# Kernel tuning notes

Hardware: AMD Instinct MI355X
Metric: run time of the kernel (lower is better)

## Reference

```python
import jax, jax.numpy as jnp
import numpy as np

EPS = 1e-5  # BatchNorm eps (torch default)

def _bn(x, mean, var, gamma, beta):
    # eval-mode BatchNorm over the trailing (heads, ch) axes
    return (x - mean) * (gamma / jnp.sqrt(var + EPS)) + beta

def setup_inputs() -> dict:
    key = jax.random.key(0)
    ks = jax.random.split(key, 8)
    B, C, W, H = 16, 256, 64, 64
    heads, k, u, m = 4, 16, 1, 23
    vv = 256
    kh, vh = k // heads, vv // heads
    x = jax.random.normal(ks[0], (B, C, W, H), dtype=jnp.float32)
    q_w = jax.random.normal(ks[1], (heads, kh, C), dtype=jnp.float32) * 0.05
    k_w = jax.random.normal(ks[2], (heads, kh * u, C), dtype=jnp.float32) * 0.05
    v_w = jax.random.normal(ks[3], (heads, vh * u, C), dtype=jnp.float32) * 0.05
    q_gamma = 0.5 + jax.random.uniform(ks[4], (heads, kh), dtype=jnp.float32)
    q_beta = jax.random.normal(ks[5], (heads, kh), dtype=jnp.float32) * 0.1
    q_mean = jnp.zeros((heads, kh), dtype=jnp.float32)
    q_var = jnp.ones((heads, kh), dtype=jnp.float32)
    k_gamma = 0.5 + jax.random.uniform(ks[6], (heads, kh * u), dtype=jnp.float32)
    k_beta = jax.random.normal(ks[7], (heads, kh * u), dtype=jnp.float32) * 0.1
    k_mean = jnp.zeros((heads, kh * u), dtype=jnp.float32)
    k_var = jnp.ones((heads, kh * u), dtype=jnp.float32)
    embedding = jax.random.normal(jax.random.fold_in(key, 99), (kh, heads, u, 1, m, m), dtype=jnp.float32) * 0.05
    return {"x": x, "q_w": q_w, "q_gamma": q_gamma, "q_beta": q_beta, "q_mean": q_mean,
            "q_var": q_var, "k_w": k_w, "k_gamma": k_gamma, "k_beta": k_beta,
            "k_mean": k_mean, "k_var": k_var, "v_w": v_w, "embedding": embedding}

def reference(x, q_w, q_gamma, q_beta, q_mean, q_var, k_w, k_gamma, k_beta, k_mean, k_var, v_w, embedding):
    B, C, W, H = x.shape
    heads, kh, _ = q_w.shape
    u = embedding.shape[2]
    m = embedding.shape[-1]
    vh = v_w.shape[1] // u
    pad = (m - 1) // 2

    # 1x1 conv projections (all heads stacked) -> channels-last
    q = jnp.einsum('bcxy,hkc->bxyhk', x, q_w)                      # [B,W,H,heads,kh]
    q = _bn(q, q_mean, q_var, q_gamma, q_beta)
    kk = jnp.einsum('bcxy,hkc->bxyhk', x, k_w)                     # [B,W,H,heads,kh*u]
    kk = _bn(kk, k_mean, k_var, k_gamma, k_beta)
    # softmax over all spatial positions, per (head, key-channel)
    sm = jax.nn.softmax(kk.reshape(B, W * H, heads, kh * u), axis=1)
    sm = sm.reshape(B, W, H, heads, kh, u)                          # [B,W,H,h,kh,u]
    v = jnp.einsum('bcxy,hvc->bxyhv', x, v_w).reshape(B, W, H, heads, vh, u)

    # content lambda: sum over all spatial positions
    lambda_c = jnp.einsum('bxyhku,bxyhvu->bhkv', sm, v)             # [B,h,kh,vh]
    y_c = jnp.einsum('bxyhk,bhkv->bxyhv', q, lambda_c)              # [B,W,H,h,vh]

    # positional lambda via grouped 2D conv (conv3d kernel depth is 1 -> 2D conv per vh slice)
    v_conv = v.transpose(0, 4, 3, 5, 1, 2).reshape(B * vh, heads * u, W, H)
    w = jnp.squeeze(embedding, axis=3).transpose(1, 0, 2, 3, 4).reshape(heads * kh, u, m, m)
    conv = jax.lax.conv_general_dilated(
        v_conv, w, window_strides=(1, 1), padding=[(pad, pad), (pad, pad)],
        dimension_numbers=('NCHW', 'OIHW', 'NCHW'), feature_group_count=heads)
    # [B*vh, heads*kh, W, H] -> sum over spatial (matches .sum(dim=[1,2]) in source)
    lambda_p = conv.reshape(B, vh, heads, kh, W, H).sum(axis=(4, 5))
    lambda_p = lambda_p.transpose(0, 2, 3, 1)                       # [B,h,kh,vh]
    y_p = jnp.einsum('bxyhk,bhkv->bxyhv', q, lambda_p)

    out = (y_c + y_p).reshape(B, W, H, heads * vh).transpose(0, 3, 1, 2)  # [B,vv,W,H]
    return out
```

## Files before the change

kernel.cpp:

```cpp
#include <hip/hip_runtime.h>
#include <math.h>

#define C_   256
#define WH   4096

typedef _Float16 f16x8 __attribute__((ext_vector_type(8)));
typedef float    f32x4 __attribute__((ext_vector_type(4)));


__global__ __launch_bounds__(512) void proj_kernel(
    const float* __restrict__ x,
    const float* __restrict__ qw, const float* __restrict__ kw,
    const float* __restrict__ qg, const float* __restrict__ qb,
    const float* __restrict__ qm, const float* __restrict__ qv,
    const float* __restrict__ kg, const float* __restrict__ kb,
    const float* __restrict__ km, const float* __restrict__ kv,
    const float* __restrict__ emb,
    float* __restrict__ qbn, float* __restrict__ kkbn,
    float* __restrict__ pstats, float* __restrict__ Wt)
{
    if (blockIdx.x >= 256) {
        int wb = blockIdx.x - 256;
        int hk = wb >> 2, quarter = wb & 3;
        int h = hk >> 2, k = hk & 3;
        const float* e = emb + (size_t)(k * 4 + h) * 529;
        __shared__ float colsum[23][64];
        for (int t2 = threadIdx.x; t2 < 23 * 64; t2 += 512) {
            int i = t2 / 64, q = t2 % 64;
            int jlo = max(0, q - 52), jhi = min(22, q + 11);
            float s = 0.f;
            for (int j = jlo; j <= jhi; ++j) s += e[i * 23 + j];
            colsum[i][q] = s;
        }
        __syncthreads();
        for (int tt = threadIdx.x; tt < 1024; tt += 512) {
            int t2 = quarter * 1024 + tt;
            int p = t2 >> 6, q = t2 & 63;
            int ilo = max(0, p - 52), ihi = min(22, p + 11);
            float s = 0.f;
            for (int i = ilo; i <= ihi; ++i) s += colsum[i][q];
            Wt[(size_t)hk * WH + t2] = s;
        }
        return;
    }

    int t = threadIdx.x;
    int b = blockIdx.x >> 4, chunk = blockIdx.x & 15;
    int lane = t & 63;
    int og = __builtin_amdgcn_readfirstlane(t >> 6);
    int isK = og >> 2;
    int o4 = (og & 3) * 4;
    int xy = chunk * 256 + lane * 4;

    const float* wsrc = isK ? kw : qw;
    const float* w0 = wsrc + (size_t)(o4 + 0) * 256;
    const float* w1 = wsrc + (size_t)(o4 + 1) * 256;
    const float* w2 = wsrc + (size_t)(o4 + 2) * 256;
    const float* w3 = wsrc + (size_t)(o4 + 3) * 256;

    float4 a0 = {0,0,0,0}, a1 = {0,0,0,0}, a2 = {0,0,0,0}, a3 = {0,0,0,0};
    const float* xb = x + (size_t)b * C_ * WH + xy;
#pragma unroll 8
    for (int c = 0; c < 256; ++c) {
        float4 xv = *(const float4*)(xb + (size_t)c * WH);
        float f0 = w0[c], f1 = w1[c], f2 = w2[c], f3 = w3[c];
        a0.x += xv.x*f0; a0.y += xv.y*f0; a0.z += xv.z*f0; a0.w += xv.w*f0;
        a1.x += xv.x*f1; a1.y += xv.y*f1; a1.z += xv.z*f1; a1.w += xv.w*f1;
        a2.x += xv.x*f2; a2.y += xv.y*f2; a2.z += xv.z*f2; a2.w += xv.w*f2;
        a3.x += xv.x*f3; a3.y += xv.y*f3; a3.z += xv.z*f3; a3.w += xv.w*f3;
    }
    float4 acc4[4] = {a0, a1, a2, a3};

    if (!isK) {
#pragma unroll
        for (int i = 0; i < 4; ++i) {
            int hk = o4 + i;
            float s  = qg[hk] * rsqrtf(qv[hk] + 1e-5f);
            float tq = qb[hk] - qm[hk] * s;
            float4 a = acc4[i], o;
            o.x = a.x * s + tq; o.y = a.y * s + tq;
            o.z = a.z * s + tq; o.w = a.w * s + tq;
            *(float4*)(qbn + ((size_t)b * 16 + hk) * WH + xy) = o;
        }
    } else {
#pragma unroll
        for (int i = 0; i < 4; ++i) {
            int hk = o4 + i;
            float s2 = kg[hk] * rsqrtf(kv[hk] + 1e-5f);
            float tk = kb[hk] - km[hk] * s2;
            float4 a = acc4[i], o;
            o.x = a.x * s2 + tk; o.y = a.y * s2 + tk;
            o.z = a.z * s2 + tk; o.w = a.w * s2 + tk;
            *(float4*)(kkbn + ((size_t)b * 16 + hk) * WH + xy) = o;
            float m = fmaxf(fmaxf(o.x, o.y), fmaxf(o.z, o.w));
#pragma unroll
            for (int off = 32; off; off >>= 1) m = fmaxf(m, __shfl_xor(m, off, 64));
            float e = __expf(o.x - m) + __expf(o.y - m) + __expf(o.z - m) + __expf(o.w - m);
#pragma unroll
            for (int off = 32; off; off >>= 1) e += __shfl_xor(e, off, 64);
            if (lane == 0) {
                float* ps = pstats + ((size_t)(b * 16 + hk) * 16 + chunk) * 2;
                ps[0] = m; ps[1] = e;
            }
        }
    }
}

__global__ __launch_bounds__(512) void ut_kernel(
    const float* __restrict__ x, const float* __restrict__ kkbn,
    const float* __restrict__ pstats, const float* __restrict__ Wt,
    float* __restrict__ Mpart)
{
    __shared__ _Float16 xls[256][72];
    __shared__ _Float16 wls[32][72];
    __shared__ float st[32];
    int t = threadIdx.x;
    int b = blockIdx.x >> 5, s5 = blockIdx.x & 31;
    int xys0 = s5 * 128;
    int lane = t & 63;
    int wid = __builtin_amdgcn_readfirstlane(t >> 6);
    int r16 = lane & 15, g = lane >> 4;
    int n0 = wid * 32;

    if (t < 16) {
        const float* ps = pstats + (size_t)(b * 16 + t) * 32;
        float M = ps[0];
#pragma unroll
        for (int ch = 1; ch < 16; ++ch) M = fmaxf(M, ps[ch * 2]);
        float S = 0.f;
#pragma unroll
        for (int ch = 0; ch < 16; ++ch) S += ps[ch * 2 + 1] * __expf(ps[ch * 2] - M);
        st[2 * t]     = M;
        st[2 * t + 1] = 1.f / S;
    }

    int sc = t >> 1, shalf = t & 1;
    int wr = t >> 3, wco = (t & 7) * 8;

    f32x4 acc00 = {0.f,0.f,0.f,0.f}, acc01 = {0.f,0.f,0.f,0.f};
    f32x4 acc10 = {0.f,0.f,0.f,0.f}, acc11 = {0.f,0.f,0.f,0.f};

    for (int ch = 0; ch < 2; ++ch) {
        int kbase = xys0 + ch * 64;
        __syncthreads();
        {
            const float* xp = x + ((size_t)b * C_ + sc) * WH + kbase + shalf * 32;
#pragma unroll
            for (int j = 0; j < 4; ++j) {
                float4 u  = *(const float4*)(xp + j * 8);
                float4 u2 = *(const float4*)(xp + j * 8 + 4);
                f16x8 o;
                o[0] = (_Float16)u.x;  o[1] = (_Float16)u.y;
                o[2] = (_Float16)u.z;  o[3] = (_Float16)u.w;
                o[4] = (_Float16)u2.x; o[5] = (_Float16)u2.y;
                o[6] = (_Float16)u2.z; o[7] = (_Float16)u2.w;
                *(f16x8*)&xls[sc][shalf * 32 + j * 8] = o;
            }
        }
        if (t < 256) {
            f16x8 o;
            if (wr < 16) {
                float wm   = st[2 * wr];
                float winv = st[2 * wr + 1];
                const float* src = kkbn + ((size_t)b * 16 + wr) * WH + kbase + wco;
                float4 u  = *(const float4*)(src);
                float4 u2 = *(const float4*)(src + 4);
                o[0] = (_Float16)(__expf(u.x  - wm) * winv);
                o[1] = (_Float16)(__expf(u.y  - wm) * winv);
                o[2] = (_Float16)(__expf(u.z  - wm) * winv);
                o[3] = (_Float16)(__expf(u.w  - wm) * winv);
                o[4] = (_Float16)(__expf(u2.x - wm) * winv);
                o[5] = (_Float16)(__expf(u2.y - wm) * winv);
                o[6] = (_Float16)(__expf(u2.z - wm) * winv);
                o[7] = (_Float16)(__expf(u2.w - wm) * winv);
            } else {
                const float* src = Wt + (size_t)(wr - 16) * WH + kbase + wco;
                float4 u  = *(const float4*)(src);
                float4 u2 = *(const float4*)(src + 4);
                o[0] = (_Float16)u.x;  o[1] = (_Float16)u.y;
                o[2] = (_Float16)u.z;  o[3] = (_Float16)u.w;
                o[4] = (_Float16)u2.x; o[5] = (_Float16)u2.y;
                o[6] = (_Float16)u2.z; o[7] = (_Float16)u2.w;
            }
            *(f16x8*)&wls[wr][wco] = o;
        }
        __syncthreads();
#pragma unroll
        for (int s = 0; s < 2; ++s) {
            int koff = s * 32 + g * 8;
            f16x8 A0 = *(const f16x8*)&wls[r16     ][koff];
            f16x8 A1 = *(const f16x8*)&wls[16 + r16][koff];
            f16x8 B0 = *(const f16x8*)&xls[n0 + r16     ][koff];
            f16x8 B1 = *(const f16x8*)&xls[n0 + 16 + r16][koff];
            acc00 = __builtin_amdgcn_mfma_f32_16x16x32_f16(A0, B0, acc00, 0, 0, 0);
            acc01 = __builtin_amdgcn_mfma_f32_16x16x32_f16(A0, B1, acc01, 0, 0, 0);
            acc10 = __builtin_amdgcn_mfma_f32_16x16x32_f16(A1, B0, acc10, 0, 0, 0);
            acc11 = __builtin_amdgcn_mfma_f32_16x16x32_f16(A1, B1, acc11, 0, 0, 0);
        }
    }

    float* mp = Mpart + (size_t)(b * 32 + s5) * 8192;
    int colA = n0 + r16, colB = n0 + 16 + r16;
    int row0 = g * 4, row1 = 16 + g * 4;
#pragma unroll
    for (int rr = 0; rr < 4; ++rr) {
        mp[(row0 + rr) * 256 + colA] = acc00[rr];
        mp[(row0 + rr) * 256 + colB] = acc01[rr];
        mp[(row1 + rr) * 256 + colA] = acc10[rr];
        mp[(row1 + rr) * 256 + colB] = acc11[rr];
    }
}

__global__ __launch_bounds__(256) void lam_kernel(
    const float* __restrict__ Mpart, const float* __restrict__ vw,
    float* __restrict__ lam)
{
    __shared__ float msum[256];
    __shared__ float vls[64][68];
    __shared__ float psum[4][64];
    int t = threadIdx.x;
    int b = blockIdx.x >> 4, hk = blockIdx.x & 15, h = hk >> 2;

    {
        const float* mp = Mpart + (size_t)b * 32 * 8192 + t;
        float s = 0.f;
        for (int seg = 0; seg < 32; ++seg) {
            const float* m2 = mp + (size_t)seg * 8192;
            s += m2[hk * 256] + m2[(16 + hk) * 256];
        }
        msum[t] = s;
    }

    int v = t & 63, cq = t >> 6;
    float acc = 0.f;
    const float* vwh = vw + (size_t)h * 64 * 256;
    for (int ch = 0; ch < 4; ++ch) {
        __syncthreads();
#pragma unroll
        for (int k = 0; k < 4; ++k) {
            int e = t + k * 256;
            int vv = e >> 4, c4 = (e & 15) * 4;
            *(float4*)&vls[vv][c4] = *(const float4*)(vwh + (size_t)vv * 256 + ch * 64 + c4);
        }
        __syncthreads();
#pragma unroll
        for (int i4 = 0; i4 < 4; ++i4) {
            float4 a  = *(const float4*)&vls[v][cq * 16 + i4 * 4];
            float4 m4 = *(const float4*)&msum[ch * 64 + cq * 16 + i4 * 4];
            acc += a.x * m4.x + a.y * m4.y + a.z * m4.z + a.w * m4.w;
        }
    }
    psum[cq][v] = acc;
    __syncthreads();
    if (t < 64)
        lam[((size_t)b * 16 + hk) * 64 + t] =
            psum[0][t] + psum[1][t] + psum[2][t] + psum[3][t];
}

__global__ __launch_bounds__(256) void out_kernel(
    const float* __restrict__ qbn, const float* __restrict__ lam,
    float* __restrict__ out)
{
    int t = threadIdx.x;
    int b = blockIdx.x >> 4, s = blockIdx.x & 15;
    int h = s >> 2, qc = s & 3;
    int xy = qc * 1024 + t * 4;
    float4 q0 = *(const float4*)(qbn + ((size_t)b * 16 + h * 4 + 0) * WH + xy);
    float4 q1 = *(const float4*)(qbn + ((size_t)b * 16 + h * 4 + 1) * WH + xy);
    float4 q2 = *(const float4*)(qbn + ((size_t)b * 16 + h * 4 + 2) * WH + xy);
    float4 q3 = *(const float4*)(qbn + ((size_t)b * 16 + h * 4 + 3) * WH + xy);
    const float* lb = lam + (size_t)b * 1024 + (size_t)h * 256;
    float* ob = out + ((size_t)b * 256 + (size_t)h * 64) * WH + xy;
#pragma unroll 8
    for (int v = 0; v < 64; ++v) {
        float l0 = lb[v], l1 = lb[64 + v], l2 = lb[128 + v], l3 = lb[192 + v];
        float4 o;
        o.x = q0.x*l0 + q1.x*l1 + q2.x*l2 + q3.x*l3;
        o.y = q0.y*l0 + q1.y*l1 + q2.y*l2 + q3.y*l3;
        o.z = q0.z*l0 + q1.z*l1 + q2.z*l2 + q3.z*l3;
        o.w = q0.w*l0 + q1.w*l1 + q2.w*l2 + q3.w*l3;
        *(float4*)(ob + (size_t)v * WH) = o;
    }
}

extern "C" void kernel_launch(void* const* d_in, const int* in_sizes, int n_in,
                              void* d_out, int out_size, void* d_ws, size_t ws_size,
                              hipStream_t stream)
{
    const float* x   = (const float*)d_in[0];
    const float* qw  = (const float*)d_in[1];
    const float* qg  = (const float*)d_in[2];
    const float* qb  = (const float*)d_in[3];
    const float* qm  = (const float*)d_in[4];
    const float* qv  = (const float*)d_in[5];
    const float* kw  = (const float*)d_in[6];
    const float* kg  = (const float*)d_in[7];
    const float* kb  = (const float*)d_in[8];
    const float* km  = (const float*)d_in[9];
    const float* kv  = (const float*)d_in[10];
    const float* vw  = (const float*)d_in[11];
    const float* emb = (const float*)d_in[12];

    float* ws     = (float*)d_ws;
    float* qbn    = ws;
    float* kkbn   = ws + 1048576;
    float* pstats = ws + 2097152;
    float* Wt     = ws + 2105344;
    float* Mpart  = ws + 2170880;
    float* lam    = ws + 6365184;
    float* out    = (float*)d_out;

    hipLaunchKernelGGL(proj_kernel,  dim3(320), dim3(512), 0, stream,
                       x, qw, kw, qg, qb, qm, qv, kg, kb, km, kv, emb,
                       qbn, kkbn, pstats, Wt);
    hipLaunchKernelGGL(ut_kernel,    dim3(512), dim3(512), 0, stream,
                       x, kkbn, pstats, Wt, Mpart);
    hipLaunchKernelGGL(lam_kernel,   dim3(256), dim3(256), 0, stream, Mpart, vw, lam);
    hipLaunchKernelGGL(out_kernel,   dim3(256), dim3(256), 0, stream, qbn, lam, out);
}
```

Before: 74.48 us.

## Fuse lambda reduction into ut_kernel with atomic accumulation, drop lam_kernel

The lam_kernel and the Mpart scratch buffer are removed. Each ut_kernel block now sums its MFMA partial tiles in shared memory, multiplies them by v_w directly and atomically adds its partial lambda into a lam buffer. That buffer is zeroed by the extra blocks of proj_kernel. This removes a kernel launch and the write and re-read of a partials buffer of about 16 MB, at the cost of float atomics (order-dependent rounding) and v_w being re-read from global or L2 by every block.

```diff
diff --git a/kernel.cpp b/kernel.cpp
--- a/kernel.cpp
+++ b/kernel.cpp
@@ -17,10 +17,12 @@
     const float* __restrict__ km, const float* __restrict__ kv,
     const float* __restrict__ emb,
     float* __restrict__ qbn, float* __restrict__ kkbn,
-    float* __restrict__ pstats, float* __restrict__ Wt)
+    float* __restrict__ pstats, float* __restrict__ Wt,
+    float* __restrict__ lam)
 {
     if (blockIdx.x >= 256) {
         int wb = blockIdx.x - 256;
+        if (threadIdx.x < 256) lam[wb * 256 + threadIdx.x] = 0.f;
         int hk = wb >> 2, quarter = wb & 3;
         int h = hk >> 2, k = hk & 3;
         const float* e = emb + (size_t)(k * 4 + h) * 529;
@@ -109,11 +111,12 @@
 __global__ __launch_bounds__(512) void ut_kernel(
     const float* __restrict__ x, const float* __restrict__ kkbn,
     const float* __restrict__ pstats, const float* __restrict__ Wt,
-    float* __restrict__ Mpart)
+    const float* __restrict__ vw, float* __restrict__ lam)
 {
     __shared__ _Float16 xls[256][72];
     __shared__ _Float16 wls[32][72];
     __shared__ float st[32];
+    __shared__ float msum[16][260];
     int t = threadIdx.x;
     int b = blockIdx.x >> 5, s5 = blockIdx.x & 31;
     int xys0 = s5 * 128;
@@ -199,62 +202,36 @@
         }
     }
 
-    float* mp = Mpart + (size_t)(b * 32 + s5) * 8192;
-    int colA = n0 + r16, colB = n0 + 16 + r16;
-    int row0 = g * 4, row1 = 16 + g * 4;
-#pragma unroll
-    for (int rr = 0; rr < 4; ++rr) {
-        mp[(row0 + rr) * 256 + colA] = acc00[rr];
-        mp[(row0 + rr) * 256 + colB] = acc01[rr];
-        mp[(row1 + rr) * 256 + colA] = acc10[rr];
-        mp[(row1 + rr) * 256 + colB] = acc11[rr];
-    }
-}
-
-__global__ __launch_bounds__(256) void lam_kernel(
-    const float* __restrict__ Mpart, const float* __restrict__ vw,
-    float* __restrict__ lam)
-{
-    __shared__ float msum[256];
-    __shared__ float vls[64][68];
-    __shared__ float psum[4][64];
-    int t = threadIdx.x;
-    int b = blockIdx.x >> 4, hk = blockIdx.x & 15, h = hk >> 2;
-
     {
-        const float* mp = Mpart + (size_t)b * 32 * 8192 + t;
-        float s = 0.f;
-        for (int seg = 0; seg < 32; ++seg) {
-            const float* m2 = mp + (size_t)seg * 8192;
-            s += m2[hk * 256] + m2[(16 + hk) * 256];
-        }
-        msum[t] = s;
-    }
-
-    int v = t & 63, cq = t >> 6;
-    float acc = 0.f;
-    const float* vwh = vw + (size_t)h * 64 * 256;
-    for (int ch = 0; ch < 4; ++ch) {
-        __syncthreads();
-#pragma unroll
-        for (int k = 0; k < 4; ++k) {
-            int e = t + k * 256;
-            int vv = e >> 4, c4 = (e & 15) * 4;
-            *(float4*)&vls[vv][c4] = *(const float4*)(vwh + (size_t)vv * 256 + ch * 64 + c4);
-        }
-        __syncthreads();
-#pragma unroll
-        for (int i4 = 0; i4 < 4; ++i4) {
-            float4 a  = *(const float4*)&vls[v][cq * 16 + i4 * 4];
-            float4 m4 = *(const float4*)&msum[ch * 64 + cq * 16 + i4 * 4];
-            acc += a.x * m4.x + a.y * m4.y + a.z * m4.z + a.w * m4.w;
-        }
-    }
-    psum[cq][v] = acc;
+        int colA = n0 + r16, colB = n0 + 16 + r16;
+        int row0 = g * 4;
+#pragma unroll
+        for (int rr = 0; rr < 4; ++rr) {
+            msum[row0 + rr][colA] = acc00[rr] + acc10[rr];
+            msum[row0 + rr][colB] = acc01[rr] + acc11[rr];
+        }
+    }
     __syncthreads();
-    if (t < 64)
-        lam[((size_t)b * 16 + hk) * 64 + t] =
-            psum[0][t] + psum[1][t] + psum[2][t] + psum[3][t];
+
+    {
+        int r = t >> 5;
+        int v = t & 31;
+        int h = r >> 2;
+        const float* vwa = vw + ((size_t)h * 64 + v) * 256;
+        const float* vwb = vwa + 32 * 256;
+        float la = 0.f, lb2 = 0.f;
+#pragma unroll 8
+        for (int c4 = 0; c4 < 64; ++c4) {
+            float4 m4 = *(const float4*)&msum[r][c4 * 4];
+            float4 wa = *(const float4*)(vwa + c4 * 4);
+            float4 wb = *(const float4*)(vwb + c4 * 4);
+            la  += m4.x*wa.x + m4.y*wa.y + m4.z*wa.z + m4.w*wa.w;
+            lb2 += m4.x*wb.x + m4.y*wb.y + m4.z*wb.z + m4.w*wb.w;
+        }
+        float* lp = lam + ((size_t)b * 16 + r) * 64 + v;
+        atomicAdd(lp,      la);
+        atomicAdd(lp + 32, lb2);
+    }
 }
 
 __global__ __launch_bounds__(256) void out_kernel(
@@ -306,15 +283,13 @@
     float* kkbn   = ws + 1048576;
     float* pstats = ws + 2097152;
     float* Wt     = ws + 2105344;
-    float* Mpart  = ws + 2170880;
-    float* lam    = ws + 6365184;
+    float* lam    = ws + 2170880;
     float* out    = (float*)d_out;
 
     hipLaunchKernelGGL(proj_kernel,  dim3(320), dim3(512), 0, stream,
                        x, qw, kw, qg, qb, qm, qv, kg, kb, km, kv, emb,
-                       qbn, kkbn, pstats, Wt);
+                       qbn, kkbn, pstats, Wt, lam);
     hipLaunchKernelGGL(ut_kernel,    dim3(512), dim3(512), 0, stream,
-                       x, kkbn, pstats, Wt, Mpart);
-    hipLaunchKernelGGL(lam_kernel,   dim3(256), dim3(256), 0, stream, Mpart, vw, lam);
+                       x, kkbn, pstats, Wt, vw, lam);
     hipLaunchKernelGGL(out_kernel,   dim3(256), dim3(256), 0, stream, qbn, lam, out);
 }
```

Result: slower. 121.5 us (+63.1%).

## Compute q and k projections per thread and drop softmax max-subtraction

Applied to the files above, without the earlier changes.

The projection kernel now has each thread compute both the q and the k projection for one pixel, 4 channels each, in 1024-thread blocks. It loads x once for both, where before separate q and k wave groups each read it with float4. The k softmax no longer subtracts a running max: exp is taken directly in the projection kernel and summed into a per-(batch, channel) total with atomicAdd, and the ut kernel only scales by the reciprocal of that sum. This removes the partial-stats pass and the exp work in the ut kernel, and halves x reads in projection. In exchange it adds a memset, atomics, scalar rather than vector loads, and a risk of overflow for large logits.

```diff
diff --git a/kernel.cpp b/kernel.cpp
--- a/kernel.cpp
+++ b/kernel.cpp
@@ -8,7 +8,7 @@
 typedef float    f32x4 __attribute__((ext_vector_type(4)));
 
 
-__global__ __launch_bounds__(512) void proj_kernel(
+__global__ __launch_bounds__(1024) void proj_kernel(
     const float* __restrict__ x,
     const float* __restrict__ qw, const float* __restrict__ kw,
     const float* __restrict__ qg, const float* __restrict__ qb,
@@ -16,8 +16,8 @@
     const float* __restrict__ kg, const float* __restrict__ kb,
     const float* __restrict__ km, const float* __restrict__ kv,
     const float* __restrict__ emb,
-    float* __restrict__ qbn, float* __restrict__ kkbn,
-    float* __restrict__ pstats, float* __restrict__ Wt)
+    float* __restrict__ qbn, float* __restrict__ ebn,
+    float* __restrict__ S, float* __restrict__ Wt)
 {
     if (blockIdx.x >= 256) {
         int wb = blockIdx.x - 256;
@@ -25,7 +25,7 @@
         int h = hk >> 2, k = hk & 3;
         const float* e = emb + (size_t)(k * 4 + h) * 529;
         __shared__ float colsum[23][64];
-        for (int t2 = threadIdx.x; t2 < 23 * 64; t2 += 512) {
+        for (int t2 = threadIdx.x; t2 < 23 * 64; t2 += 1024) {
             int i = t2 / 64, q = t2 % 64;
             int jlo = max(0, q - 52), jhi = min(22, q + 11);
             float s = 0.f;
@@ -33,8 +33,8 @@
             colsum[i][q] = s;
         }
         __syncthreads();
-        for (int tt = threadIdx.x; tt < 1024; tt += 512) {
-            int t2 = quarter * 1024 + tt;
+        {
+            int t2 = quarter * 1024 + threadIdx.x;
             int p = t2 >> 6, q = t2 & 63;
             int ilo = max(0, p - 52), ihi = min(22, p + 11);
             float s = 0.f;
@@ -46,74 +46,57 @@
 
     int t = threadIdx.x;
     int b = blockIdx.x >> 4, chunk = blockIdx.x & 15;
+    int px = t & 255;
     int lane = t & 63;
-    int og = __builtin_amdgcn_readfirstlane(t >> 6);
-    int isK = og >> 2;
-    int o4 = (og & 3) * 4;
-    int xy = chunk * 256 + lane * 4;
-
-    const float* wsrc = isK ? kw : qw;
-    const float* w0 = wsrc + (size_t)(o4 + 0) * 256;
-    const float* w1 = wsrc + (size_t)(o4 + 1) * 256;
-    const float* w2 = wsrc + (size_t)(o4 + 2) * 256;
-    const float* w3 = wsrc + (size_t)(o4 + 3) * 256;
-
-    float4 a0 = {0,0,0,0}, a1 = {0,0,0,0}, a2 = {0,0,0,0}, a3 = {0,0,0,0};
+    int og = __builtin_amdgcn_readfirstlane(t >> 8);
+    int o4 = og * 4;
+    int xy = chunk * 256 + px;
+
+    const float* wq0 = qw + (size_t)(o4 + 0) * 256;
+    const float* wq1 = qw + (size_t)(o4 + 1) * 256;
+    const float* wq2 = qw + (size_t)(o4 + 2) * 256;
+    const float* wq3 = qw + (size_t)(o4 + 3) * 256;
+    const float* wk0 = kw + (size_t)(o4 + 0) * 256;
+    const float* wk1 = kw + (size_t)(o4 + 1) * 256;
+    const float* wk2 = kw + (size_t)(o4 + 2) * 256;
+    const float* wk3 = kw + (size_t)(o4 + 3) * 256;
+
+    float accq[4] = {0.f, 0.f, 0.f, 0.f};
+    float acck[4] = {0.f, 0.f, 0.f, 0.f};
     const float* xb = x + (size_t)b * C_ * WH + xy;
 #pragma unroll 8
     for (int c = 0; c < 256; ++c) {
-        float4 xv = *(const float4*)(xb + (size_t)c * WH);
-        float f0 = w0[c], f1 = w1[c], f2 = w2[c], f3 = w3[c];
-        a0.x += xv.x*f0; a0.y += xv.y*f0; a0.z += xv.z*f0; a0.w += xv.w*f0;
-        a1.x += xv.x*f1; a1.y += xv.y*f1; a1.z += xv.z*f1; a1.w += xv.w*f1;
-        a2.x += xv.x*f2; a2.y += xv.y*f2; a2.z += xv.z*f2; a2.w += xv.w*f2;
-        a3.x += xv.x*f3; a3.y += xv.y*f3; a3.z += xv.z*f3; a3.w += xv.w*f3;
-    }
-    float4 acc4[4] = {a0, a1, a2, a3};
-
-    if (!isK) {
-#pragma unroll
-        for (int i = 0; i < 4; ++i) {
-            int hk = o4 + i;
-            float s  = qg[hk] * rsqrtf(qv[hk] + 1e-5f);
-            float tq = qb[hk] - qm[hk] * s;
-            float4 a = acc4[i], o;
-            o.x = a.x * s + tq; o.y = a.y * s + tq;
-            o.z = a.z * s + tq; o.w = a.w * s + tq;
-            *(float4*)(qbn + ((size_t)b * 16 + hk) * WH + xy) = o;
-        }
-    } else {
-#pragma unroll
-        for (int i = 0; i < 4; ++i) {
-            int hk = o4 + i;
-            float s2 = kg[hk] * rsqrtf(kv[hk] + 1e-5f);
-            float tk = kb[hk] - km[hk] * s2;
-            float4 a = acc4[i], o;
-            o.x = a.x * s2 + tk; o.y = a.y * s2 + tk;
-            o.z = a.z * s2 + tk; o.w = a.w * s2 + tk;
-            *(float4*)(kkbn + ((size_t)b * 16 + hk) * WH + xy) = o;
-            float m = fmaxf(fmaxf(o.x, o.y), fmaxf(o.z, o.w));
-#pragma unroll
-            for (int off = 32; off; off >>= 1) m = fmaxf(m, __shfl_xor(m, off, 64));
-            float e = __expf(o.x - m) + __expf(o.y - m) + __expf(o.z - m) + __expf(o.w - m);
-#pragma unroll
-            for (int off = 32; off; off >>= 1) e += __shfl_xor(e, off, 64);
-            if (lane == 0) {
-                float* ps = pstats + ((size_t)(b * 16 + hk) * 16 + chunk) * 2;
-                ps[0] = m; ps[1] = e;
-            }
-        }
+        float xv = xb[(size_t)c * WH];
+        accq[0] += xv * wq0[c]; accq[1] += xv * wq1[c];
+        accq[2] += xv * wq2[c]; accq[3] += xv * wq3[c];
+        acck[0] += xv * wk0[c]; acck[1] += xv * wk1[c];
+        acck[2] += xv * wk2[c]; acck[3] += xv * wk3[c];
+    }
+#pragma unroll
+    for (int i = 0; i < 4; ++i) {
+        int hk = o4 + i;
+        float s  = qg[hk] * rsqrtf(qv[hk] + 1e-5f);
+        float tq = qb[hk] - qm[hk] * s;
+        float s2 = kg[hk] * rsqrtf(kv[hk] + 1e-5f);
+        float tk = kb[hk] - km[hk] * s2;
+        qbn[((size_t)b * 16 + hk) * WH + xy] = accq[i] * s + tq;
+        float e = __expf(acck[i] * s2 + tk);
+        ebn[((size_t)b * 16 + hk) * WH + xy] = e;
+        float ssum = e;
+#pragma unroll
+        for (int off = 32; off; off >>= 1) ssum += __shfl_xor(ssum, off, 64);
+        if (lane == 0) atomicAdd(&S[b * 16 + hk], ssum);
     }
 }
 
 __global__ __launch_bounds__(512) void ut_kernel(
-    const float* __restrict__ x, const float* __restrict__ kkbn,
-    const float* __restrict__ pstats, const float* __restrict__ Wt,
+    const float* __restrict__ x, const float* __restrict__ ebn,
+    const float* __restrict__ S, const float* __restrict__ Wt,
     float* __restrict__ Mpart)
 {
     __shared__ _Float16 xls[256][72];
     __shared__ _Float16 wls[32][72];
-    __shared__ float st[32];
+    __shared__ float st[16];
     int t = threadIdx.x;
     int b = blockIdx.x >> 5, s5 = blockIdx.x & 31;
     int xys0 = s5 * 128;
@@ -122,17 +105,7 @@
     int r16 = lane & 15, g = lane >> 4;
     int n0 = wid * 32;
 
-    if (t < 16) {
-        const float* ps = pstats + (size_t)(b * 16 + t) * 32;
-        float M = ps[0];
-#pragma unroll
-        for (int ch = 1; ch < 16; ++ch) M = fmaxf(M, ps[ch * 2]);
-        float S = 0.f;
-#pragma unroll
-        for (int ch = 0; ch < 16; ++ch) S += ps[ch * 2 + 1] * __expf(ps[ch * 2] - M);
-        st[2 * t]     = M;
-        st[2 * t + 1] = 1.f / S;
-    }
+    if (t < 16) st[t] = 1.f / S[b * 16 + t];
 
     int sc = t >> 1, shalf = t & 1;
     int wr = t >> 3, wco = (t & 7) * 8;
@@ -158,30 +131,17 @@
             }
         }
         if (t < 256) {
+            const float* src = (wr < 16)
+                ? ebn + ((size_t)b * 16 + wr) * WH + kbase + wco
+                : Wt + (size_t)(wr - 16) * WH + kbase + wco;
+            float scale = (wr < 16) ? st[wr] : 1.f;
+            float4 u  = *(const float4*)(src);
+            float4 u2 = *(const float4*)(src + 4);
             f16x8 o;
-            if (wr < 16) {
-                float wm   = st[2 * wr];
-                float winv = st[2 * wr + 1];
-                const float* src = kkbn + ((size_t)b * 16 + wr) * WH + kbase + wco;
-                float4 u  = *(const float4*)(src);
-                float4 u2 = *(const float4*)(src + 4);
-                o[0] = (_Float16)(__expf(u.x  - wm) * winv);
-                o[1] = (_Float16)(__expf(u.y  - wm) * winv);
-                o[2] = (_Float16)(__expf(u.z  - wm) * winv);
-                o[3] = (_Float16)(__expf(u.w  - wm) * winv);
-                o[4] = (_Float16)(__expf(u2.x - wm) * winv);
-                o[5] = (_Float16)(__expf(u2.y - wm) * winv);
-                o[6] = (_Float16)(__expf(u2.z - wm) * winv);
-                o[7] = (_Float16)(__expf(u2.w - wm) * winv);
-            } else {
-                const float* src = Wt + (size_t)(wr - 16) * WH + kbase + wco;
-                float4 u  = *(const float4*)(src);
-                float4 u2 = *(const float4*)(src + 4);
-                o[0] = (_Float16)u.x;  o[1] = (_Float16)u.y;
-                o[2] = (_Float16)u.z;  o[3] = (_Float16)u.w;
-                o[4] = (_Float16)u2.x; o[5] = (_Float16)u2.y;
-                o[6] = (_Float16)u2.z; o[7] = (_Float16)u2.w;
-            }
+            o[0] = (_Float16)(u.x  * scale); o[1] = (_Float16)(u.y  * scale);
+            o[2] = (_Float16)(u.z  * scale); o[3] = (_Float16)(u.w  * scale);
+            o[4] = (_Float16)(u2.x * scale); o[5] = (_Float16)(u2.y * scale);
+            o[6] = (_Float16)(u2.z * scale); o[7] = (_Float16)(u2.w * scale);
             *(f16x8*)&wls[wr][wco] = o;
         }
         __syncthreads();
@@ -301,20 +261,21 @@
     const float* vw  = (const float*)d_in[11];
     const float* emb = (const float*)d_in[12];
 
-    float* ws     = (float*)d_ws;
-    float* qbn    = ws;
-    float* kkbn   = ws + 1048576;
-    float* pstats = ws + 2097152;
-    float* Wt     = ws + 2105344;
-    float* Mpart  = ws + 2170880;
-    float* lam    = ws + 6365184;
-    float* out    = (float*)d_out;
-
-    hipLaunchKernelGGL(proj_kernel,  dim3(320), dim3(512), 0, stream,
+    float* ws    = (float*)d_ws;
+    float* qbn   = ws;
+    float* ebn   = ws + 1048576;
+    float* Sv    = ws + 2097152;
+    float* Wt    = ws + 2097408;
+    float* Mpart = ws + 2162944;
+    float* lam   = ws + 6357248;
+    float* out   = (float*)d_out;
+
+    hipMemsetAsync(Sv, 0, 256 * sizeof(float), stream);
+    hipLaunchKernelGGL(proj_kernel,  dim3(320), dim3(1024), 0, stream,
                        x, qw, kw, qg, qb, qm, qv, kg, kb, km, kv, emb,
-                       qbn, kkbn, pstats, Wt);
+                       qbn, ebn, Sv, Wt);
     hipLaunchKernelGGL(ut_kernel,    dim3(512), dim3(512), 0, stream,
-                       x, kkbn, pstats, Wt, Mpart);
+                       x, ebn, Sv, Wt, Mpart);
     hipLaunchKernelGGL(lam_kernel,   dim3(256), dim3(256), 0, stream, Mpart, vw, lam);
     hipLaunchKernelGGL(out_kernel,   dim3(256), dim3(256), 0, stream, qbn, lam, out);
 }
```

New measurement: 105.1 us. 1.41x slower.

## Retile projection to 8 outputs x 2 pixels per thread; pre-sum MFMA halves

Applied to the files above, without the earlier changes.

The projection kernel now gives each thread 8 output channels over 2 pixels instead of 4 channels over 4 pixels. Each loaded x element is therefore reused across more weights, and the per-wave softmax partial stats double to 32 chunks per row. The ut kernel adds its two accumulator halves before writing Mpart, which halves that buffer and the reads in lam_kernel. The cost is more scalar weight loads per channel iteration and a longer stats reduction.

```diff
diff --git a/kernel.cpp b/kernel.cpp
--- a/kernel.cpp
+++ b/kernel.cpp
@@ -44,62 +44,65 @@
         return;
     }
 
-    int t = threadIdx.x;
+    int t = threadIdx.x, lane = t & 63;
+    int w8 = __builtin_amdgcn_readfirstlane(t >> 6);
+    int half = w8 >> 2;
+    int rg = w8 & 3;
+    int isK = rg >> 1;
+    int r0 = (rg & 1) * 8;
     int b = blockIdx.x >> 4, chunk = blockIdx.x & 15;
-    int lane = t & 63;
-    int og = __builtin_amdgcn_readfirstlane(t >> 6);
-    int isK = og >> 2;
-    int o4 = (og & 3) * 4;
-    int xy = chunk * 256 + lane * 4;
+    int xy = chunk * 256 + half * 128 + lane * 2;
 
     const float* wsrc = isK ? kw : qw;
-    const float* w0 = wsrc + (size_t)(o4 + 0) * 256;
-    const float* w1 = wsrc + (size_t)(o4 + 1) * 256;
-    const float* w2 = wsrc + (size_t)(o4 + 2) * 256;
-    const float* w3 = wsrc + (size_t)(o4 + 3) * 256;
-
-    float4 a0 = {0,0,0,0}, a1 = {0,0,0,0}, a2 = {0,0,0,0}, a3 = {0,0,0,0};
+    const float* w0 = wsrc + (size_t)(r0 + 0) * 256;
+    const float* w1 = wsrc + (size_t)(r0 + 1) * 256;
+    const float* w2 = wsrc + (size_t)(r0 + 2) * 256;
+    const float* w3 = wsrc + (size_t)(r0 + 3) * 256;
+    const float* w4 = wsrc + (size_t)(r0 + 4) * 256;
+    const float* w5 = wsrc + (size_t)(r0 + 5) * 256;
+    const float* w6 = wsrc + (size_t)(r0 + 6) * 256;
+    const float* w7 = wsrc + (size_t)(r0 + 7) * 256;
+
+    float2 a0 = {0,0}, a1 = {0,0}, a2 = {0,0}, a3 = {0,0};
+    float2 a4 = {0,0}, a5 = {0,0}, a6 = {0,0}, a7 = {0,0};
     const float* xb = x + (size_t)b * C_ * WH + xy;
 #pragma unroll 8
     for (int c = 0; c < 256; ++c) {
-        float4 xv = *(const float4*)(xb + (size_t)c * WH);
+        float2 xv = *(const float2*)(xb + (size_t)c * WH);
         float f0 = w0[c], f1 = w1[c], f2 = w2[c], f3 = w3[c];
-        a0.x += xv.x*f0; a0.y += xv.y*f0; a0.z += xv.z*f0; a0.w += xv.w*f0;
-        a1.x += xv.x*f1; a1.y += xv.y*f1; a1.z += xv.z*f1; a1.w += xv.w*f1;
-        a2.x += xv.x*f2; a2.y += xv.y*f2; a2.z += xv.z*f2; a2.w += xv.w*f2;
-        a3.x += xv.x*f3; a3.y += xv.y*f3; a3.z += xv.z*f3; a3.w += xv.w*f3;
-    }
-    float4 acc4[4] = {a0, a1, a2, a3};
+        float f4 = w4[c], f5 = w5[c], f6 = w6[c], f7 = w7[c];
+        a0.x += xv.x*f0; a0.y += xv.y*f0;  a1.x += xv.x*f1; a1.y += xv.y*f1;
+        a2.x += xv.x*f2; a2.y += xv.y*f2;  a3.x += xv.x*f3; a3.y += xv.y*f3;
+        a4.x += xv.x*f4; a4.y += xv.y*f4;  a5.x += xv.x*f5; a5.y += xv.y*f5;
+        a6.x += xv.x*f6; a6.y += xv.y*f6;  a7.x += xv.x*f7; a7.y += xv.y*f7;
+    }
+    float2 acc[8] = {a0, a1, a2, a3, a4, a5, a6, a7};
 
     if (!isK) {
 #pragma unroll
-        for (int i = 0; i < 4; ++i) {
-            int hk = o4 + i;
+        for (int i = 0; i < 8; ++i) {
+            int hk = r0 + i;
             float s  = qg[hk] * rsqrtf(qv[hk] + 1e-5f);
             float tq = qb[hk] - qm[hk] * s;
-            float4 a = acc4[i], o;
-            o.x = a.x * s + tq; o.y = a.y * s + tq;
-            o.z = a.z * s + tq; o.w = a.w * s + tq;
-            *(float4*)(qbn + ((size_t)b * 16 + hk) * WH + xy) = o;
+            float2 o; o.x = acc[i].x * s + tq; o.y = acc[i].y * s + tq;
+            *(float2*)(qbn + ((size_t)b * 16 + hk) * WH + xy) = o;
         }
     } else {
 #pragma unroll
-        for (int i = 0; i < 4; ++i) {
-            int hk = o4 + i;
+        for (int i = 0; i < 8; ++i) {
+            int hk = r0 + i;
             float s2 = kg[hk] * rsqrtf(kv[hk] + 1e-5f);
             float tk = kb[hk] - km[hk] * s2;
-            float4 a = acc4[i], o;
-            o.x = a.x * s2 + tk; o.y = a.y * s2 + tk;
-            o.z = a.z * s2 + tk; o.w = a.w * s2 + tk;
-            *(float4*)(kkbn + ((size_t)b * 16 + hk) * WH + xy) = o;
-            float m = fmaxf(fmaxf(o.x, o.y), fmaxf(o.z, o.w));
+            float2 o; o.x = acc[i].x * s2 + tk; o.y = acc[i].y * s2 + tk;
+            *(float2*)(kkbn + ((size_t)b * 16 + hk) * WH + xy) = o;
+            float m = fmaxf(o.x, o.y);
 #pragma unroll
             for (int off = 32; off; off >>= 1) m = fmaxf(m, __shfl_xor(m, off, 64));
-            float e = __expf(o.x - m) + __expf(o.y - m) + __expf(o.z - m) + __expf(o.w - m);
+            float e = __expf(o.x - m) + __expf(o.y - m);
 #pragma unroll
             for (int off = 32; off; off >>= 1) e += __shfl_xor(e, off, 64);
             if (lane == 0) {
-                float* ps = pstats + ((size_t)(b * 16 + hk) * 16 + chunk) * 2;
+                float* ps = pstats + ((size_t)(b * 16 + hk) * 32 + chunk * 2 + half) * 2;
                 ps[0] = m; ps[1] = e;
             }
         }
@@ -123,13 +126,13 @@
     int n0 = wid * 32;
 
     if (t < 16) {
-        const float* ps = pstats + (size_t)(b * 16 + t) * 32;
+        const float* ps = pstats + (size_t)(b * 16 + t) * 64;
         float M = ps[0];
 #pragma unroll
-        for (int ch = 1; ch < 16; ++ch) M = fmaxf(M, ps[ch * 2]);
+        for (int ch = 1; ch < 32; ++ch) M = fmaxf(M, ps[ch * 2]);
         float S = 0.f;
 #pragma unroll
-        for (int ch = 0; ch < 16; ++ch) S += ps[ch * 2 + 1] * __expf(ps[ch * 2] - M);
+        for (int ch = 0; ch < 32; ++ch) S += ps[ch * 2 + 1] * __expf(ps[ch * 2] - M);
         st[2 * t]     = M;
         st[2 * t + 1] = 1.f / S;
     }
@@ -199,15 +202,13 @@
         }
     }
 
-    float* mp = Mpart + (size_t)(b * 32 + s5) * 8192;
+    float* mp = Mpart + (size_t)(b * 32 + s5) * 4096;
     int colA = n0 + r16, colB = n0 + 16 + r16;
-    int row0 = g * 4, row1 = 16 + g * 4;
+    int row0 = g * 4;
 #pragma unroll
     for (int rr = 0; rr < 4; ++rr) {
-        mp[(row0 + rr) * 256 + colA] = acc00[rr];
-        mp[(row0 + rr) * 256 + colB] = acc01[rr];
-        mp[(row1 + rr) * 256 + colA] = acc10[rr];
-        mp[(row1 + rr) * 256 + colB] = acc11[rr];
+        mp[(row0 + rr) * 256 + colA] = acc00[rr] + acc10[rr];
+        mp[(row0 + rr) * 256 + colB] = acc01[rr] + acc11[rr];
     }
 }
 
@@ -222,12 +223,9 @@
     int b = blockIdx.x >> 4, hk = blockIdx.x & 15, h = hk >> 2;
 
     {
-        const float* mp = Mpart + (size_t)b * 32 * 8192 + t;
+        const float* mp = Mpart + (size_t)b * 32 * 4096 + hk * 256 + t;
         float s = 0.f;
-        for (int seg = 0; seg < 32; ++seg) {
-            const float* m2 = mp + (size_t)seg * 8192;
-            s += m2[hk * 256] + m2[(16 + hk) * 256];
-        }
+        for (int seg = 0; seg < 32; ++seg) s += mp[(size_t)seg * 4096];
         msum[t] = s;
     }
 
@@ -305,9 +303,9 @@
     float* qbn    = ws;
     float* kkbn   = ws + 1048576;
     float* pstats = ws + 2097152;
-    float* Wt     = ws + 2105344;
-    float* Mpart  = ws + 2170880;
-    float* lam    = ws + 6365184;
+    float* Wt     = ws + 2113536;
+    float* Mpart  = ws + 2179072;
+    float* lam    = ws + 4276224;
     float* out    = (float*)d_out;
 
     hipLaunchKernelGGL(proj_kernel,  dim3(320), dim3(512), 0, stream,
```

Measured after the change: 74.90 us. No clear change (+0.6%).
